# Optimization experiments

Measured on AMD Instinct MI355X. Metric: run time of the kernel, lower is better.

## Reference

```python
import jax, jax.numpy as jnp
import numpy as np

CONF_THRESH = 0.05      # confidence_threshold
IOU_THRESH = 0.15       # nms_iou_threshold
MAX_PER_CLASS = 550     # max_detection_per_class
MAX_TOTAL = 1100        # max_detection
NEG = -1e9              # sentinel for suppressed / below-threshold scores


def _to_corners(b):
    # convert_to_min_max_corner: (cx, cy, w, h) -> (x1, y1, x2, y2)
    xy, wh = b[..., :2], b[..., 2:4]
    return jnp.concatenate([xy - wh * 0.5, xy + wh * 0.5], axis=-1)


def _area(b):
    return jnp.clip(b[..., 2] - b[..., 0], 0.0) * jnp.clip(b[..., 3] - b[..., 1], 0.0)


def _iou_one_many(box, boxes):
    # box: [4], boxes: [N,4] in corner format
    lt = jnp.maximum(box[:2], boxes[:, :2])
    rb = jnp.minimum(box[2:], boxes[:, 2:])
    wh = jnp.clip(rb - lt, 0.0)
    inter = wh[:, 0] * wh[:, 1]
    union = _area(box) + _area(boxes) - inter
    return inter / jnp.maximum(union, 1e-8)


def _nms_single(boxes, scores):
    # Exact greedy hard-NMS for one (image, class): boxes [N,4], scores [N]
    s0 = jnp.where(scores > CONF_THRESH, scores, NEG)

    def step(s, _):
        i = jnp.argmax(s)
        sc = s[i]
        suppress = _iou_one_many(boxes[i], boxes) > IOU_THRESH
        ns = jnp.where(suppress, NEG, s).at[i].set(NEG)
        return ns, (i, sc)

    _, (sel_idx, sel_score) = jax.lax.scan(step, s0, None, length=MAX_PER_CLASS)
    return sel_idx, sel_score  # [K], [K]


def _decode(predictions):
    boxes = _to_corners(predictions[:, :, :4])          # [B,N,4]
    cls_probs = jax.nn.sigmoid(predictions[:, :, 4:])   # [B,N,C]
    scores = jnp.transpose(cls_probs, (0, 2, 1))        # [B,C,N]

    nms = jax.vmap(jax.vmap(_nms_single, in_axes=(None, 0)), in_axes=(0, 0))
    sel_idx, sel_score = nms(boxes, scores)             # [B,C,K]
    B, C, K = sel_score.shape

    gboxes = jnp.take_along_axis(boxes[:, None, :, :], sel_idx[..., None], axis=2)  # [B,C,K,4]
    classes = jnp.broadcast_to(jnp.arange(C, dtype=jnp.float32)[None, :, None], (B, C, K))

    fb = gboxes.reshape(B, C * K, 4)
    fs = sel_score.reshape(B, C * K)
    fc = classes.reshape(B, C * K)

    k = min(MAX_TOTAL, C * K)
    top_s, top_i = jax.lax.top_k(fs, k)                 # combined cross-class top-k
    tb = jnp.take_along_axis(fb, top_i[..., None], axis=1)
    tc = jnp.take_along_axis(fc, top_i, axis=1)

    valid = top_s > 0.5 * NEG                           # real detections have score in (conf, 1]
    nmsed_boxes = jnp.where(valid[..., None], tb, 0.0)
    nmsed_scores = jnp.where(valid, top_s, 0.0)
    nmsed_classes = jnp.where(valid, tc, 0.0)
    valid_detections = jnp.sum(valid, axis=1).astype(jnp.int32)
    return nmsed_boxes, nmsed_scores, nmsed_classes, valid_detections


def setup_inputs() -> dict:
    key = jax.random.key(0)
    k1, k2, k3 = jax.random.split(key, 3)
    B, N, C, IMG = 4, 49104, 2, 512.0
    u = jax.random.uniform(k1, (B, N, 4), dtype=jnp.float32)
    cxcy = u[..., :2] * IMG                  # centers within the image
    wh = 16.0 + u[..., 2:] * 128.0           # plausible anchor-ish sizes
    logits = jax.random.normal(k2, (B, N, C), dtype=jnp.float32) * 1.5 - 3.0
    predictions = jnp.concatenate([cxcy, wh, logits], axis=-1)  # [B,N,6]
    images = jax.random.uniform(k3, (B, 512, 512, 3), dtype=jnp.float32)
    return {"images": images, "predictions": predictions}


def reference(images, predictions):
    # images is accepted (as in the Keras layer) but unused by the math
    return _decode(predictions)
```

## Files before the change

### kernel.cpp

```cpp
#include <hip/hip_runtime.h>
#include <stdint.h>

#define NEGV    (-1000000000.0f)
#define CONF    0.05f
#define MAXSEL  550
#define CAP     32768
#define HEAD    1024
#define HW      (HEAD / 64)
#define NBINS   4096
#define BINBASE 0xC07F0000u
#define GCAP    3072
#define NSEG    64
#define TROUNDS 3

typedef unsigned long long u64;
typedef unsigned int u32;

__device__ __forceinline__ float areaf(float4 b) {
    return __fmul_rn(fmaxf(__fsub_rn(b.z, b.x), 0.0f), fmaxf(__fsub_rn(b.w, b.y), 0.0f));
}

__device__ __forceinline__ bool iou_gt2(float4 a, float aA, float4 b, float aB) {
    float ltx = fmaxf(a.x, b.x), lty = fmaxf(a.y, b.y);
    float rbx = fminf(a.z, b.z), rby = fminf(a.w, b.w);
    float wx = fmaxf(__fsub_rn(rbx, ltx), 0.0f);
    float wy = fmaxf(__fsub_rn(rby, lty), 0.0f);
    float inter = __fmul_rn(wx, wy);
    float uni = fmaxf(__fsub_rn(__fadd_rn(aA, aB), inter), 1e-8f);
    const double M = (double)0.15f + 0x1p-27;
    return (double)inter > M * (double)uni;
}

__device__ __forceinline__ u32 binof(u32 keyhi) {
    u32 bin = (keyhi - BINBASE) >> 14;
    return bin > (NBINS - 1) ? (NBINS - 1) : bin;
}

__global__ void k_decode(const float* __restrict__ pred, float4* __restrict__ boxes,
                         u32* __restrict__ hist, u32* __restrict__ llen,
                         u32* __restrict__ S_arr, u32* __restrict__ Sold,
                         int BN, int NBC) {
    int t = blockIdx.x * 256 + threadIdx.x;
    if (t < 2 * NBC * NBINS) hist[t] = 0;
    if (t < 2 * NBC) llen[t] = 0;
    if (t < NBC) { S_arr[t] = 0; Sold[t] = 0; }
    if (t >= BN) return;
    const float* p = pred + (size_t)t * 6;
    float cx = p[0], cy = p[1], w = p[2], h = p[3];
    float hw = __fmul_rn(w, 0.5f), hh = __fmul_rn(h, 0.5f);
    float4 b;
    b.x = __fsub_rn(cx, hw);
    b.y = __fsub_rn(cy, hh);
    b.z = __fadd_rn(cx, hw);
    b.w = __fadd_rn(cy, hh);
    boxes[t] = b;
}

__global__ __launch_bounds__(256) void k_hist(const float* __restrict__ pred,
                                              u32* __restrict__ hist,
                                              u64* __restrict__ L0,
                                              u32* __restrict__ llen0,
                                              int Nn, int Cc, int TIL) {
    int bt = blockIdx.x;
    int tile = bt % TIL, bc = bt / TIL;
    int b = bc / Cc, c = bc % Cc;
    int n = tile * 256 + threadIdx.x;
    bool p = false; u32 hi = 0;
    if (n < Nn) {
        float lg = pred[((size_t)b * Nn + n) * 6 + 4 + c];
        float sc = __fdiv_rn(1.0f, __fadd_rn(1.0f, expf(-lg)));
        if (sc > CONF) {
            p = true;
            hi = ~__float_as_uint(sc);
            atomicAdd(&hist[bc * NBINS + binof(hi)], 1u);
        }
    }
    u64 bal = __ballot(p);
    __shared__ u32 wb[4]; __shared__ u32 base;
    int lane = threadIdx.x & 63, wv = threadIdx.x >> 6;
    if (lane == 0) wb[wv] = (u32)__popcll(bal);
    __syncthreads();
    if (threadIdx.x == 0) {
        u32 run = 0;
        for (int q = 0; q < 4; ++q) { u32 v = wb[q]; wb[q] = run; run += v; }
        base = run ? atomicAdd(&llen0[bc], run) : 0u;
    }
    __syncthreads();
    if (p) {
        u32 pos = base + wb[wv] + (u32)__popcll(bal & ((1ull << lane) - 1ull));
        if (pos < CAP)
            L0[(size_t)bc * CAP + pos] = ((u64)hi << 32) | (u32)n;
    }
}

__global__ __launch_bounds__(1024) void k_headsort(const u64* __restrict__ list,
                                                   const u32* __restrict__ llen_cur,
                                                   const u32* __restrict__ hc,
                                                   u32* __restrict__ hn,
                                                   u32* __restrict__ ln,
                                                   const float4* __restrict__ boxes,
                                                   const u32* __restrict__ S_arr,
                                                   u64* __restrict__ headkey,
                                                   float4* __restrict__ headbox,
                                                   float* __restrict__ headarea,
                                                   u32* __restrict__ hl_arr,
                                                   u64* __restrict__ hmax_arr,
                                                   int Nn, int Cc) {
    int bc = blockIdx.x, b = bc / Cc;
    int tid = threadIdx.x, lane = tid & 63, wv = tid >> 6;
    __shared__ u64 buf[4096];
    __shared__ u32 gcnt;
    __shared__ int s_t;
    for (int i = tid; i < NBINS; i += 1024) hn[bc * NBINS + i] = 0;
    if (tid == 0) { ln[bc] = 0; gcnt = 0; }
    __syncthreads();
    if ((int)S_arr[bc] >= MAXSEL) { if (tid == 0) hl_arr[bc] = 0; return; }
    int len = (int)llen_cur[bc]; if (len > CAP) len = CAP;
    if (wv == 0) {
        if (lane == 0) s_t = -1;
        const u32* h = hc + bc * NBINS;
        int base = lane * 64;
        u32 s = 0;
        for (int i = 0; i < 64; ++i) s += h[base + i];
        u32 p = s;
        for (int d = 1; d < 64; d <<= 1) { u32 o = __shfl_up(p, d); if (lane >= d) p += o; }
        u32 total = __shfl(p, 63);
        u32 K = total < HEAD ? total : HEAD;
        if (K > 0) {
            u64 bal = __ballot(p >= K);
            int tl = (int)__builtin_ctzll(bal);
            if (lane == tl) {
                u32 cum = p - s;
                for (int i = 0; i < 64; ++i) {
                    cum += h[base + i];
                    if (cum >= K) {
                        s_t = (cum <= GCAP) ? (base + i) : (base + i - 1);
                        break;
                    }
                }
            }
        }
    }
    __syncthreads();
    int t = s_t;
    if (t >= 0) {
        const u64* src = list + (size_t)bc * CAP;
        for (int i = tid; i < len; i += 1024) {
            u64 key = src[i];
            if ((int)binof((u32)(key >> 32)) <= t) {
                u32 pos = atomicAdd(&gcnt, 1u);
                if (pos < GCAP) buf[pos] = key;
            }
        }
    }
    __syncthreads();
    int g = (int)gcnt; if (g > GCAP) g = GCAP;
    int SN = 1; while (SN < g) SN <<= 1;
    for (int i = g + tid; i < SN; i += 1024) buf[i] = ~0ull;
    __syncthreads();
    for (int k = 2; k <= SN; k <<= 1) {
        for (int j = k >> 1; j > 0; j >>= 1) {
            for (int idx = tid; idx < SN / 2; idx += 1024) {
                int i = ((idx & ~(j - 1)) << 1) | (idx & (j - 1));
                int q = i | j;
                bool up = ((i & k) == 0);
                u64 x = buf[i], y = buf[q];
                if ((x > y) == up) { buf[i] = y; buf[q] = x; }
            }
            __syncthreads();
        }
    }
    int hl = g < HEAD ? g : HEAD;
    if (tid == 0) { hl_arr[bc] = (u32)hl; hmax_arr[bc] = hl > 0 ? buf[hl - 1] : 0ull; }
    for (int i = tid; i < hl; i += 1024) {
        u64 key = buf[i];
        headkey[bc * HEAD + i] = key;
        float4 bx = boxes[(size_t)b * Nn + (u32)key];
        headbox[bc * HEAD + i] = bx;
        headarea[bc * HEAD + i] = areaf(bx);
    }
}

__global__ __launch_bounds__(256) void k_premask(const float4* __restrict__ headbox,
                                                 const float* __restrict__ headarea,
                                                 const u32* __restrict__ hl_arr,
                                                 u64* __restrict__ masks) {
    int blk = blockIdx.x, bc = blk >> 4, rb = blk & 15;
    int hl = (int)hl_arr[bc];
    if (hl <= 0) return;
    __shared__ float4 chB[HEAD];
    __shared__ float  chA[HEAD];
    for (int i = threadIdx.x; i < hl; i += 256) {
        chB[i] = headbox[bc * HEAD + i];
        chA[i] = headarea[bc * HEAD + i];
    }
    __syncthreads();
    int r = (rb << 6) + (threadIdx.x & 63);
    int part = threadIdx.x >> 6;
    if (r >= hl) return;
    float4 a = chB[r]; float aA = chA[r];
    u64* row = masks + ((size_t)bc * HEAD + r) * HW;
    for (int w = part * 4; w < part * 4 + 4; ++w) {
        u64 bits = 0;
        int cb = w << 6;
        int j1 = hl - cb; if (j1 > 64) j1 = 64;
        int j0 = (cb > r) ? 0 : (r + 1 - cb);
        for (int j = j0; j < j1; ++j)
            if (iou_gt2(a, aA, chB[cb + j], chA[cb + j])) bits |= (1ull << j);
        row[w] = bits;
    }
}

__global__ __launch_bounds__(1024) void k_chain(const u64* __restrict__ headkey,
                                                const u32* __restrict__ hl_arr,
                                                const u64* __restrict__ masks,
                                                const float4* __restrict__ headbox,
                                                const float* __restrict__ headarea,
                                                u32* __restrict__ sel_n,
                                                float* __restrict__ sel_s,
                                                float4* __restrict__ selb_g,
                                                float* __restrict__ sela_g,
                                                u32* __restrict__ S_arr,
                                                u32* __restrict__ Sold) {
    int bc = blockIdx.x;
    int tid = threadIdx.x, lane = tid & 63;
    __shared__ u64 mrow[HEAD * HW];
    __shared__ u64 kky[HEAD];
    __shared__ u32 selidx[MAXSEL];
    __shared__ int s_S;
    int S0 = (int)S_arr[bc];
    if (tid == 0) Sold[bc] = (u32)S0;
    int hl = (int)hl_arr[bc];
    if (hl <= 0 || S0 >= MAXSEL) return;
    const u64* gm = masks + (size_t)bc * HEAD * HW;
    for (int i = tid; i < hl * HW; i += 1024) mrow[i] = gm[i];
    for (int i = tid; i < hl; i += 1024) kky[i] = headkey[bc * HEAD + i];
    __syncthreads();
    if (tid < 64) {
        u64 rem = ~0ull;
        if (lane < HW) {
            int lo = lane << 6;
            rem = (hl >= lo + 64) ? 0ull : (hl <= lo ? ~0ull : ~((1ull << (hl - lo)) - 1ull));
        }
        int S = S0;
        while (S < MAXSEL) {
            bool av = (lane < HW) && (rem != ~0ull);
            u64 bal = __ballot(av);
            if (!bal) break;
            int w0 = (int)__builtin_ctzll(bal);
            u64 nz = __shfl((u64)(~rem), w0);
            int kz = (int)__builtin_ctzll(nz);
            int i = (w0 << 6) + kz;
            if (lane == 0) selidx[S] = (u32)i;
            if (lane < HW) rem |= mrow[i * HW + lane];
            if (lane == w0) rem |= (1ull << kz);
            ++S;
        }
        if (lane == 0) { s_S = S; S_arr[bc] = (u32)S; }
    }
    __syncthreads();
    int S = s_S;
    for (int s = S0 + tid; s < S; s += 1024) {
        u32 i = selidx[s];
        u64 k64 = kky[i];
        sel_n[bc * MAXSEL + s] = (u32)k64;
        sel_s[bc * MAXSEL + s] = __uint_as_float(~(u32)(k64 >> 32));
        selb_g[bc * MAXSEL + s] = headbox[bc * HEAD + i];
        sela_g[bc * MAXSEL + s] = headarea[bc * HEAD + i];
    }
}

__global__ __launch_bounds__(256) void k_mark(const float4* __restrict__ boxes,
                                              const u64* __restrict__ Lc,
                                              const u32* __restrict__ llen_c,
                                              const float4* __restrict__ selb_g,
                                              const float* __restrict__ sela_g,
                                              const u32* __restrict__ S_arr,
                                              const u32* __restrict__ Sold,
                                              const u64* __restrict__ hmax_arr,
                                              const u32* __restrict__ hl_arr,
                                              u64* __restrict__ Ln,
                                              u32* __restrict__ llen_n,
                                              u32* __restrict__ hist_n,
                                              int Nn, int Cc) {
    int blk = blockIdx.x, bc = blk / NSEG, seg = blk % NSEG;
    int tid = threadIdx.x, lane = tid & 63, wv = tid >> 6;
    int b = bc / Cc;
    int S0 = (int)Sold[bc], S1 = (int)S_arr[bc];
    if (S1 >= MAXSEL) return;
    int len = (int)llen_c[bc]; if (len > CAP) len = CAP;
    if (len <= 0) return;
    int ns = S1 - S0;
    u64 hmax = ((int)hl_arr[bc] > 0) ? hmax_arr[bc] : 0ull;
    __shared__ float4 sb[MAXSEL];
    __shared__ float  sa[MAXSEL];
    for (int s = tid; s < ns; s += 256) {
        sb[s] = selb_g[bc * MAXSEL + S0 + s];
        sa[s] = sela_g[bc * MAXSEL + S0 + s];
    }
    __syncthreads();
    __shared__ u32 wb[4]; __shared__ u32 base;
    int chunk = (len + NSEG - 1) / NSEG;
    int lo = seg * chunk, hi2 = lo + chunk; if (hi2 > len) hi2 = len;
    const u64* src = Lc + (size_t)bc * CAP;
    u64* dst = Ln + (size_t)bc * CAP;
    for (int st = lo; st < hi2; st += 256) {
        int i = st + tid;
        bool alive = i < hi2; u64 key = 0;
        if (alive) {
            key = src[i];
            if (key <= hmax) alive = false;
            else {
                float4 bx = boxes[(size_t)b * Nn + (u32)key];
                float aA = areaf(bx);
                for (int s = 0; s < ns; ++s)
                    if (iou_gt2(bx, aA, sb[s], sa[s])) { alive = false; break; }
            }
        }
        u64 bal = __ballot(alive);
        if (lane == 0) wb[wv] = (u32)__popcll(bal);
        __syncthreads();
        if (tid == 0) {
            u32 run = 0;
            for (int q = 0; q < 4; ++q) { u32 v = wb[q]; wb[q] = run; run += v; }
            base = run ? atomicAdd(&llen_n[bc], run) : 0u;
        }
        __syncthreads();
        if (alive) {
            u32 pos = base + wb[wv] + (u32)__popcll(bal & ((1ull << lane) - 1ull));
            if (pos < CAP) dst[pos] = key;
            atomicAdd(&hist_n[bc * NBINS + binof((u32)(key >> 32))], 1u);
        }
        __syncthreads();
    }
}

__global__ __launch_bounds__(1024) void k_final(const u32* __restrict__ selcnt,
                                                const u32* __restrict__ sel_n,
                                                const float* __restrict__ sel_s,
                                                const float4* __restrict__ boxes,
                                                float* __restrict__ out,
                                                int Nn, int Cc, int Bb) {
    int b = blockIdx.x, tid = threadIdx.x;
    const int TOT = MAXSEL * 2;
    __shared__ u64 sk[2048];
    u32 c0 = selcnt[b * Cc + 0];
    u32 c1 = selcnt[b * Cc + 1];
    for (int t = tid; t < 2048; t += 1024) {
        u64 key;
        if (t < TOT) {
            int c = t / MAXSEL, k2 = t % MAXSEL;
            u32 cc = (c == 0) ? c0 : c1;
            float sc = (k2 < (int)cc) ? sel_s[(size_t)(b * Cc + c) * MAXSEL + k2] : NEGV;
            u32 u = __float_as_uint(sc);
            u32 ord = (u & 0x80000000u) ? ~u : (u | 0x80000000u);
            key = (((u64)(~ord)) << 32) | (u32)t;
        } else {
            key = ~0ull;
        }
        sk[t] = key;
    }
    __syncthreads();
    for (int k = 2; k <= 2048; k <<= 1) {
        for (int j = k >> 1; j > 0; j >>= 1) {
            int idx = tid;
            int i = ((idx & ~(j - 1)) << 1) | (idx & (j - 1));
            int p = i | j;
            bool up = ((i & k) == 0);
            u64 x = sk[i], y = sk[p];
            if ((x > y) == up) { sk[i] = y; sk[p] = x; }
            __syncthreads();
        }
    }
    int off_scores = Bb * TOT * 4;
    int off_classes = off_scores + Bb * TOT;
    int off_valid = off_classes + Bb * TOT;
    for (int r = tid; r < TOT; r += 1024) {
        u64 key = sk[r];
        u32 flat = (u32)(key & 0xffffffffull);
        u32 hi = (u32)(key >> 32);
        u32 ord = ~hi;
        float sc = (ord & 0x80000000u) ? __uint_as_float(ord & 0x7fffffffu)
                                       : __uint_as_float(~ord);
        bool valid = sc > -5.0e8f;
        int c = (int)(flat / MAXSEL), k2 = (int)(flat % MAXSEL);
        float4 bxv = make_float4(0.f, 0.f, 0.f, 0.f);
        float so = 0.f, co = 0.f;
        if (valid) {
            u32 n = sel_n[(size_t)(b * Cc + c) * MAXSEL + k2];
            bxv = boxes[(size_t)b * Nn + n];
            so = sc;
            co = (float)c;
        }
        ((float4*)out)[b * TOT + r] = bxv;
        out[off_scores + b * TOT + r] = so;
        out[off_classes + b * TOT + r] = co;
    }
    if (tid == 0) out[off_valid + b] = (float)(c0 + c1);
}

extern "C" void kernel_launch(void* const* d_in, const int* in_sizes, int n_in,
                              void* d_out, int out_size, void* d_ws, size_t ws_size,
                              hipStream_t stream) {
    const float* pred = (const float*)d_in[1];
    float* out = (float*)d_out;
    int Bb = out_size / 6601;
    int Nn = in_sizes[1] / (6 * Bb);
    const int Cc = 2;
    if (Bb <= 0 || Nn <= 0) return;
    int NBC = Bb * Cc;
    int TIL = (Nn + 255) / 256;

    char* ws = (char*)d_ws;
    size_t off = 0;
    auto alloc = [&](size_t bytes) { void* p = ws + off; off = (off + bytes + 255) & ~(size_t)255; return p; };
    float4* boxes   = (float4*)alloc((size_t)Bb * Nn * 16);
    u64* L0         = (u64*)alloc((size_t)NBC * CAP * 8);
    u64* L1         = (u64*)alloc((size_t)NBC * CAP * 8);
    u32* hist       = (u32*)alloc(2 * (size_t)NBC * NBINS * 4);
    u32* llen       = (u32*)alloc(2 * NBC * 4);
    u64* headkey    = (u64*)alloc((size_t)NBC * HEAD * 8);
    float4* headbox = (float4*)alloc((size_t)NBC * HEAD * 16);
    float* headarea = (float*)alloc((size_t)NBC * HEAD * 4);
    u32* hl_arr     = (u32*)alloc(NBC * 4);
    u64* hmax_arr   = (u64*)alloc(NBC * 8);
    u32* sel_n      = (u32*)alloc((size_t)NBC * MAXSEL * 4);
    float* sel_s    = (float*)alloc((size_t)NBC * MAXSEL * 4);
    float4* selb_g  = (float4*)alloc((size_t)NBC * MAXSEL * 16);
    float* sela_g   = (float*)alloc((size_t)NBC * MAXSEL * 4);
    u32* S_arr      = (u32*)alloc(NBC * 4);
    u32* Sold       = (u32*)alloc(NBC * 4);
    u64* masks      = (u64*)alloc((size_t)NBC * HEAD * HW * 8);
    if (off > ws_size) return;

    int BN = Bb * Nn;
    k_decode<<<(BN + 255) / 256, 256, 0, stream>>>(pred, boxes, hist, llen, S_arr, Sold, BN, NBC);
    k_hist<<<NBC * TIL, 256, 0, stream>>>(pred, hist, L0, llen, Nn, Cc, TIL);

    for (int r = 0; r < TROUNDS; ++r) {
        int cur = r & 1, nxt = (r + 1) & 1;
        u64* Lc = cur ? L1 : L0;
        u64* Ln = nxt ? L1 : L0;
        u32* lc = llen + cur * NBC;
        u32* ln = llen + nxt * NBC;
        u32* hc = hist + (size_t)cur * NBC * NBINS;
        u32* hn = hist + (size_t)nxt * NBC * NBINS;
        k_headsort<<<NBC, 1024, 0, stream>>>(Lc, lc, hc, hn, ln, boxes, S_arr,
                                             headkey, headbox, headarea, hl_arr, hmax_arr, Nn, Cc);
        k_premask<<<NBC * 16, 256, 0, stream>>>(headbox, headarea, hl_arr, masks);
        k_chain<<<NBC, 1024, 0, stream>>>(headkey, hl_arr, masks, headbox, headarea,
                                          sel_n, sel_s, selb_g, sela_g, S_arr, Sold);
        if (r + 1 < TROUNDS)
            k_mark<<<NBC * NSEG, 256, 0, stream>>>(boxes, Lc, lc, selb_g, sela_g, S_arr, Sold,
                                                   hmax_arr, hl_arr, Ln, ln, hn, Nn, Cc);
    }
    k_final<<<Bb, 1024, 0, stream>>>(S_arr, sel_n, sel_s, boxes, out, Nn, Cc, Bb);
}
```

Baseline: 359.2 us.

## Fuse all NMS stages into one persistent cooperative kernel with grid syncs

Replaces the sequence of separate launches (decode, histogram, per-round headsort, premask, chain, mark, final) with a single cooperative mega-kernel of 256 blocks of 1024 threads. Stages are separated by grid.sync() and share a union of shared-memory buffers. The goal is to remove the launch overhead and inter-kernel gaps of about a dozen small launches. In exchange, the serial stages (sort, chain) run on only a few blocks while the rest of the grid waits at barriers. The large 1024-thread blocks with a big shared union may also limit occupancy.

After: 749.3 us. 109% more time.

```diff
diff --git a/kernel.cpp b/kernel.cpp
--- a/kernel.cpp
+++ b/kernel.cpp
@@ -1,20 +1,55 @@
 #include <hip/hip_runtime.h>
+#include <hip/hip_cooperative_groups.h>
 #include <stdint.h>
+
+namespace cg = cooperative_groups;
 
 #define NEGV    (-1000000000.0f)
 #define CONF    0.05f
 #define MAXSEL  550
 #define CAP     32768
 #define HEAD    1024
-#define HW      (HEAD / 64)
+#define HW      16
 #define NBINS   4096
 #define BINBASE 0xC07F0000u
 #define GCAP    3072
-#define NSEG    64
+#define NSEG    32
+#define GRID    256
 #define TROUNDS 3
 
 typedef unsigned long long u64;
 typedef unsigned int u32;
+
+struct Params {
+    const float* pred;
+    float* out;
+    float4* boxes;
+    u64* L0; u64* L1;
+    u32* hist;
+    u32* llen;
+    int* tbin;
+    u64* headkey;
+    float4* headbox;
+    float* headarea;
+    u32* hl_arr;
+    u64* hmax_arr;
+    u32* sel_n;
+    float* sel_s;
+    float4* selb_g;
+    float* sela_g;
+    u32* S_arr;
+    u32* Sold;
+    u64* masks;
+    int Bb, Nn, Cc, NBC, TIL4;
+};
+
+union SharedU {
+    struct { u64 mrow[HEAD * HW]; u64 kky[HEAD]; u32 selidx[MAXSEL]; } ch;
+    struct { u64 buf[4096]; } hs;
+    struct { float4 chB[HEAD]; float chA[HEAD]; } pm;
+    struct { float4 sb[MAXSEL]; float sa[MAXSEL]; } mk;
+    struct { u64 sk[2048]; } fn;
+};
 
 __device__ __forceinline__ float areaf(float4 b) {
     return __fmul_rn(fmaxf(__fsub_rn(b.z, b.x), 0.0f), fmaxf(__fsub_rn(b.w, b.y), 0.0f));
@@ -36,367 +71,343 @@
     return bin > (NBINS - 1) ? (NBINS - 1) : bin;
 }
 
-__global__ void k_decode(const float* __restrict__ pred, float4* __restrict__ boxes,
-                         u32* __restrict__ hist, u32* __restrict__ llen,
-                         u32* __restrict__ S_arr, u32* __restrict__ Sold,
-                         int BN, int NBC) {
-    int t = blockIdx.x * 256 + threadIdx.x;
-    if (t < 2 * NBC * NBINS) hist[t] = 0;
-    if (t < 2 * NBC) llen[t] = 0;
-    if (t < NBC) { S_arr[t] = 0; Sold[t] = 0; }
-    if (t >= BN) return;
-    const float* p = pred + (size_t)t * 6;
-    float cx = p[0], cy = p[1], w = p[2], h = p[3];
-    float hw = __fmul_rn(w, 0.5f), hh = __fmul_rn(h, 0.5f);
-    float4 b;
-    b.x = __fsub_rn(cx, hw);
-    b.y = __fsub_rn(cy, hh);
-    b.z = __fadd_rn(cx, hw);
-    b.w = __fadd_rn(cy, hh);
-    boxes[t] = b;
-}
-
-__global__ __launch_bounds__(256) void k_hist(const float* __restrict__ pred,
-                                              u32* __restrict__ hist,
-                                              u64* __restrict__ L0,
-                                              u32* __restrict__ llen0,
-                                              int Nn, int Cc, int TIL) {
-    int bt = blockIdx.x;
-    int tile = bt % TIL, bc = bt / TIL;
-    int b = bc / Cc, c = bc % Cc;
-    int n = tile * 256 + threadIdx.x;
-    bool p = false; u32 hi = 0;
-    if (n < Nn) {
-        float lg = pred[((size_t)b * Nn + n) * 6 + 4 + c];
-        float sc = __fdiv_rn(1.0f, __fadd_rn(1.0f, expf(-lg)));
-        if (sc > CONF) {
-            p = true;
-            hi = ~__float_as_uint(sc);
-            atomicAdd(&hist[bc * NBINS + binof(hi)], 1u);
-        }
+__global__ void __launch_bounds__(1024, 4) mega(Params P) {
+    cg::grid_group grid = cg::this_grid();
+    __shared__ SharedU sh;
+    __shared__ u32 s_wb[16];
+    __shared__ u32 s_base, s_gcnt;
+    __shared__ int s_S;
+
+    const int tid = threadIdx.x, lane = tid & 63, wv = tid >> 6;
+    const int gsz = gridDim.x * 1024;
+    const int gt0 = blockIdx.x * 1024 + tid;
+    const int NBC = P.NBC, Cc = P.Cc, Nn = P.Nn, Bb = P.Bb;
+
+    for (int t = gt0; t < 2 * NBC * NBINS; t += gsz) P.hist[t] = 0;
+    if (gt0 < 2 * NBC) P.llen[gt0] = 0;
+    if (gt0 < NBC) { P.S_arr[gt0] = 0; P.Sold[gt0] = 0; }
+    int BN = Bb * Nn;
+    for (int t = gt0; t < BN; t += gsz) {
+        const float* p = P.pred + (size_t)t * 6;
+        float cx = p[0], cy = p[1], w = p[2], h = p[3];
+        float hw = __fmul_rn(w, 0.5f), hh = __fmul_rn(h, 0.5f);
+        float4 b;
+        b.x = __fsub_rn(cx, hw);
+        b.y = __fsub_rn(cy, hh);
+        b.z = __fadd_rn(cx, hw);
+        b.w = __fadd_rn(cy, hh);
+        P.boxes[t] = b;
     }
-    u64 bal = __ballot(p);
-    __shared__ u32 wb[4]; __shared__ u32 base;
-    int lane = threadIdx.x & 63, wv = threadIdx.x >> 6;
-    if (lane == 0) wb[wv] = (u32)__popcll(bal);
-    __syncthreads();
-    if (threadIdx.x == 0) {
-        u32 run = 0;
-        for (int q = 0; q < 4; ++q) { u32 v = wb[q]; wb[q] = run; run += v; }
-        base = run ? atomicAdd(&llen0[bc], run) : 0u;
-    }
-    __syncthreads();
-    if (p) {
-        u32 pos = base + wb[wv] + (u32)__popcll(bal & ((1ull << lane) - 1ull));
-        if (pos < CAP)
-            L0[(size_t)bc * CAP + pos] = ((u64)hi << 32) | (u32)n;
-    }
-}
-
-__global__ __launch_bounds__(1024) void k_headsort(const u64* __restrict__ list,
-                                                   const u32* __restrict__ llen_cur,
-                                                   const u32* __restrict__ hc,
-                                                   u32* __restrict__ hn,
-                                                   u32* __restrict__ ln,
-                                                   const float4* __restrict__ boxes,
-                                                   const u32* __restrict__ S_arr,
-                                                   u64* __restrict__ headkey,
-                                                   float4* __restrict__ headbox,
-                                                   float* __restrict__ headarea,
-                                                   u32* __restrict__ hl_arr,
-                                                   u64* __restrict__ hmax_arr,
-                                                   int Nn, int Cc) {
-    int bc = blockIdx.x, b = bc / Cc;
-    int tid = threadIdx.x, lane = tid & 63, wv = tid >> 6;
-    __shared__ u64 buf[4096];
-    __shared__ u32 gcnt;
-    __shared__ int s_t;
-    for (int i = tid; i < NBINS; i += 1024) hn[bc * NBINS + i] = 0;
-    if (tid == 0) { ln[bc] = 0; gcnt = 0; }
-    __syncthreads();
-    if ((int)S_arr[bc] >= MAXSEL) { if (tid == 0) hl_arr[bc] = 0; return; }
-    int len = (int)llen_cur[bc]; if (len > CAP) len = CAP;
-    if (wv == 0) {
-        if (lane == 0) s_t = -1;
-        const u32* h = hc + bc * NBINS;
-        int base = lane * 64;
-        u32 s = 0;
-        for (int i = 0; i < 64; ++i) s += h[base + i];
-        u32 p = s;
-        for (int d = 1; d < 64; d <<= 1) { u32 o = __shfl_up(p, d); if (lane >= d) p += o; }
-        u32 total = __shfl(p, 63);
-        u32 K = total < HEAD ? total : HEAD;
-        if (K > 0) {
-            u64 bal = __ballot(p >= K);
-            int tl = (int)__builtin_ctzll(bal);
-            if (lane == tl) {
-                u32 cum = p - s;
-                for (int i = 0; i < 64; ++i) {
-                    cum += h[base + i];
-                    if (cum >= K) {
-                        s_t = (cum <= GCAP) ? (base + i) : (base + i - 1);
-                        break;
-                    }
-                }
-            }
-        }
-    }
-    __syncthreads();
-    int t = s_t;
-    if (t >= 0) {
-        const u64* src = list + (size_t)bc * CAP;
-        for (int i = tid; i < len; i += 1024) {
-            u64 key = src[i];
-            if ((int)binof((u32)(key >> 32)) <= t) {
-                u32 pos = atomicAdd(&gcnt, 1u);
-                if (pos < GCAP) buf[pos] = key;
-            }
-        }
-    }
-    __syncthreads();
-    int g = (int)gcnt; if (g > GCAP) g = GCAP;
-    int SN = 1; while (SN < g) SN <<= 1;
-    for (int i = g + tid; i < SN; i += 1024) buf[i] = ~0ull;
-    __syncthreads();
-    for (int k = 2; k <= SN; k <<= 1) {
-        for (int j = k >> 1; j > 0; j >>= 1) {
-            for (int idx = tid; idx < SN / 2; idx += 1024) {
-                int i = ((idx & ~(j - 1)) << 1) | (idx & (j - 1));
-                int q = i | j;
-                bool up = ((i & k) == 0);
-                u64 x = buf[i], y = buf[q];
-                if ((x > y) == up) { buf[i] = y; buf[q] = x; }
-            }
-            __syncthreads();
-        }
-    }
-    int hl = g < HEAD ? g : HEAD;
-    if (tid == 0) { hl_arr[bc] = (u32)hl; hmax_arr[bc] = hl > 0 ? buf[hl - 1] : 0ull; }
-    for (int i = tid; i < hl; i += 1024) {
-        u64 key = buf[i];
-        headkey[bc * HEAD + i] = key;
-        float4 bx = boxes[(size_t)b * Nn + (u32)key];
-        headbox[bc * HEAD + i] = bx;
-        headarea[bc * HEAD + i] = areaf(bx);
-    }
-}
-
-__global__ __launch_bounds__(256) void k_premask(const float4* __restrict__ headbox,
-                                                 const float* __restrict__ headarea,
-                                                 const u32* __restrict__ hl_arr,
-                                                 u64* __restrict__ masks) {
-    int blk = blockIdx.x, bc = blk >> 4, rb = blk & 15;
-    int hl = (int)hl_arr[bc];
-    if (hl <= 0) return;
-    __shared__ float4 chB[HEAD];
-    __shared__ float  chA[HEAD];
-    for (int i = threadIdx.x; i < hl; i += 256) {
-        chB[i] = headbox[bc * HEAD + i];
-        chA[i] = headarea[bc * HEAD + i];
-    }
-    __syncthreads();
-    int r = (rb << 6) + (threadIdx.x & 63);
-    int part = threadIdx.x >> 6;
-    if (r >= hl) return;
-    float4 a = chB[r]; float aA = chA[r];
-    u64* row = masks + ((size_t)bc * HEAD + r) * HW;
-    for (int w = part * 4; w < part * 4 + 4; ++w) {
-        u64 bits = 0;
-        int cb = w << 6;
-        int j1 = hl - cb; if (j1 > 64) j1 = 64;
-        int j0 = (cb > r) ? 0 : (r + 1 - cb);
-        for (int j = j0; j < j1; ++j)
-            if (iou_gt2(a, aA, chB[cb + j], chA[cb + j])) bits |= (1ull << j);
-        row[w] = bits;
-    }
-}
-
-__global__ __launch_bounds__(1024) void k_chain(const u64* __restrict__ headkey,
-                                                const u32* __restrict__ hl_arr,
-                                                const u64* __restrict__ masks,
-                                                const float4* __restrict__ headbox,
-                                                const float* __restrict__ headarea,
-                                                u32* __restrict__ sel_n,
-                                                float* __restrict__ sel_s,
-                                                float4* __restrict__ selb_g,
-                                                float* __restrict__ sela_g,
-                                                u32* __restrict__ S_arr,
-                                                u32* __restrict__ Sold) {
-    int bc = blockIdx.x;
-    int tid = threadIdx.x, lane = tid & 63;
-    __shared__ u64 mrow[HEAD * HW];
-    __shared__ u64 kky[HEAD];
-    __shared__ u32 selidx[MAXSEL];
-    __shared__ int s_S;
-    int S0 = (int)S_arr[bc];
-    if (tid == 0) Sold[bc] = (u32)S0;
-    int hl = (int)hl_arr[bc];
-    if (hl <= 0 || S0 >= MAXSEL) return;
-    const u64* gm = masks + (size_t)bc * HEAD * HW;
-    for (int i = tid; i < hl * HW; i += 1024) mrow[i] = gm[i];
-    for (int i = tid; i < hl; i += 1024) kky[i] = headkey[bc * HEAD + i];
-    __syncthreads();
-    if (tid < 64) {
-        u64 rem = ~0ull;
-        if (lane < HW) {
-            int lo = lane << 6;
-            rem = (hl >= lo + 64) ? 0ull : (hl <= lo ? ~0ull : ~((1ull << (hl - lo)) - 1ull));
-        }
-        int S = S0;
-        while (S < MAXSEL) {
-            bool av = (lane < HW) && (rem != ~0ull);
-            u64 bal = __ballot(av);
-            if (!bal) break;
-            int w0 = (int)__builtin_ctzll(bal);
-            u64 nz = __shfl((u64)(~rem), w0);
-            int kz = (int)__builtin_ctzll(nz);
-            int i = (w0 << 6) + kz;
-            if (lane == 0) selidx[S] = (u32)i;
-            if (lane < HW) rem |= mrow[i * HW + lane];
-            if (lane == w0) rem |= (1ull << kz);
-            ++S;
-        }
-        if (lane == 0) { s_S = S; S_arr[bc] = (u32)S; }
-    }
-    __syncthreads();
-    int S = s_S;
-    for (int s = S0 + tid; s < S; s += 1024) {
-        u32 i = selidx[s];
-        u64 k64 = kky[i];
-        sel_n[bc * MAXSEL + s] = (u32)k64;
-        sel_s[bc * MAXSEL + s] = __uint_as_float(~(u32)(k64 >> 32));
-        selb_g[bc * MAXSEL + s] = headbox[bc * HEAD + i];
-        sela_g[bc * MAXSEL + s] = headarea[bc * HEAD + i];
-    }
-}
-
-__global__ __launch_bounds__(256) void k_mark(const float4* __restrict__ boxes,
-                                              const u64* __restrict__ Lc,
-                                              const u32* __restrict__ llen_c,
-                                              const float4* __restrict__ selb_g,
-                                              const float* __restrict__ sela_g,
-                                              const u32* __restrict__ S_arr,
-                                              const u32* __restrict__ Sold,
-                                              const u64* __restrict__ hmax_arr,
-                                              const u32* __restrict__ hl_arr,
-                                              u64* __restrict__ Ln,
-                                              u32* __restrict__ llen_n,
-                                              u32* __restrict__ hist_n,
-                                              int Nn, int Cc) {
-    int blk = blockIdx.x, bc = blk / NSEG, seg = blk % NSEG;
-    int tid = threadIdx.x, lane = tid & 63, wv = tid >> 6;
-    int b = bc / Cc;
-    int S0 = (int)Sold[bc], S1 = (int)S_arr[bc];
-    if (S1 >= MAXSEL) return;
-    int len = (int)llen_c[bc]; if (len > CAP) len = CAP;
-    if (len <= 0) return;
-    int ns = S1 - S0;
-    u64 hmax = ((int)hl_arr[bc] > 0) ? hmax_arr[bc] : 0ull;
-    __shared__ float4 sb[MAXSEL];
-    __shared__ float  sa[MAXSEL];
-    for (int s = tid; s < ns; s += 256) {
-        sb[s] = selb_g[bc * MAXSEL + S0 + s];
-        sa[s] = sela_g[bc * MAXSEL + S0 + s];
-    }
-    __syncthreads();
-    __shared__ u32 wb[4]; __shared__ u32 base;
-    int chunk = (len + NSEG - 1) / NSEG;
-    int lo = seg * chunk, hi2 = lo + chunk; if (hi2 > len) hi2 = len;
-    const u64* src = Lc + (size_t)bc * CAP;
-    u64* dst = Ln + (size_t)bc * CAP;
-    for (int st = lo; st < hi2; st += 256) {
-        int i = st + tid;
-        bool alive = i < hi2; u64 key = 0;
-        if (alive) {
-            key = src[i];
-            if (key <= hmax) alive = false;
-            else {
-                float4 bx = boxes[(size_t)b * Nn + (u32)key];
-                float aA = areaf(bx);
-                for (int s = 0; s < ns; ++s)
-                    if (iou_gt2(bx, aA, sb[s], sa[s])) { alive = false; break; }
-            }
-        }
-        u64 bal = __ballot(alive);
-        if (lane == 0) wb[wv] = (u32)__popcll(bal);
+    grid.sync();
+
+    for (int bt = blockIdx.x; bt < NBC * P.TIL4; bt += gridDim.x) {
+        int tile = bt % P.TIL4, bc = bt / P.TIL4;
+        int b = bc / Cc, c = bc % Cc;
+        int n = tile * 1024 + tid;
+        bool pz = false; u32 hi = 0;
+        if (n < Nn) {
+            float lg = P.pred[((size_t)b * Nn + n) * 6 + 4 + c];
+            float sc = __fdiv_rn(1.0f, __fadd_rn(1.0f, expf(-lg)));
+            if (sc > CONF) {
+                pz = true;
+                hi = ~__float_as_uint(sc);
+                atomicAdd(&P.hist[bc * NBINS + binof(hi)], 1u);
+            }
+        }
+        u64 bal = __ballot(pz);
+        if (lane == 0) s_wb[wv] = (u32)__popcll(bal);
         __syncthreads();
         if (tid == 0) {
             u32 run = 0;
-            for (int q = 0; q < 4; ++q) { u32 v = wb[q]; wb[q] = run; run += v; }
-            base = run ? atomicAdd(&llen_n[bc], run) : 0u;
+            for (int q = 0; q < 16; ++q) { u32 v = s_wb[q]; s_wb[q] = run; run += v; }
+            s_base = run ? atomicAdd(&P.llen[bc], run) : 0u;
         }
         __syncthreads();
-        if (alive) {
-            u32 pos = base + wb[wv] + (u32)__popcll(bal & ((1ull << lane) - 1ull));
-            if (pos < CAP) dst[pos] = key;
-            atomicAdd(&hist_n[bc * NBINS + binof((u32)(key >> 32))], 1u);
+        if (pz) {
+            u32 pos = s_base + s_wb[wv] + (u32)__popcll(bal & ((1ull << lane) - 1ull));
+            if (pos < CAP) P.L0[(size_t)bc * CAP + pos] = ((u64)hi << 32) | (u32)n;
         }
         __syncthreads();
     }
-}
-
-__global__ __launch_bounds__(1024) void k_final(const u32* __restrict__ selcnt,
-                                                const u32* __restrict__ sel_n,
-                                                const float* __restrict__ sel_s,
-                                                const float4* __restrict__ boxes,
-                                                float* __restrict__ out,
-                                                int Nn, int Cc, int Bb) {
-    int b = blockIdx.x, tid = threadIdx.x;
-    const int TOT = MAXSEL * 2;
-    __shared__ u64 sk[2048];
-    u32 c0 = selcnt[b * Cc + 0];
-    u32 c1 = selcnt[b * Cc + 1];
-    for (int t = tid; t < 2048; t += 1024) {
-        u64 key;
-        if (t < TOT) {
-            int c = t / MAXSEL, k2 = t % MAXSEL;
-            u32 cc = (c == 0) ? c0 : c1;
-            float sc = (k2 < (int)cc) ? sel_s[(size_t)(b * Cc + c) * MAXSEL + k2] : NEGV;
-            u32 u = __float_as_uint(sc);
-            u32 ord = (u & 0x80000000u) ? ~u : (u | 0x80000000u);
-            key = (((u64)(~ord)) << 32) | (u32)t;
-        } else {
-            key = ~0ull;
-        }
-        sk[t] = key;
+    grid.sync();
+
+    for (int r = 0; r < TROUNDS; ++r) {
+        const u64* Lc = (r & 1) ? P.L1 : P.L0;
+        u64* Ln = (r & 1) ? P.L0 : P.L1;
+        const u32* lc = P.llen + (r & 1) * NBC;
+        u32* ln = P.llen + ((r + 1) & 1) * NBC;
+        const u32* hc = P.hist + (size_t)(r & 1) * NBC * NBINS;
+        u32* hn = P.hist + (size_t)((r + 1) & 1) * NBC * NBINS;
+
+        if (blockIdx.x == 0) {
+            for (int i = tid; i < NBC * NBINS; i += 1024) hn[i] = 0;
+            if (tid < NBC) ln[tid] = 0;
+            if (wv < NBC) {
+                const u32* h = hc + wv * NBINS;
+                int base = lane * 64;
+                u32 s = 0;
+                for (int i = 0; i < 64; ++i) s += h[base + i];
+                u32 p = s;
+                for (int d = 1; d < 64; d <<= 1) { u32 o = __shfl_up(p, d); if (lane >= d) p += o; }
+                u32 total = __shfl(p, 63);
+                u32 K = total < HEAD ? total : HEAD;
+                if (K > 0) {
+                    u64 bal = __ballot(p >= K);
+                    int tl = (int)__builtin_ctzll(bal);
+                    if (lane == tl) {
+                        u32 cum = p - s;
+                        for (int i = 0; i < 64; ++i) {
+                            cum += h[base + i];
+                            if (cum >= K) {
+                                P.tbin[wv] = (cum <= GCAP) ? (base + i) : (base + i - 1);
+                                break;
+                            }
+                        }
+                    }
+                } else if (lane == 0) P.tbin[wv] = -1;
+            }
+        }
+        grid.sync();
+
+        if (blockIdx.x < NBC) {
+            int bc = blockIdx.x, b = bc / Cc;
+            if (tid == 0) s_gcnt = 0;
+            __syncthreads();
+            if ((int)P.S_arr[bc] >= MAXSEL) {
+                if (tid == 0) P.hl_arr[bc] = 0;
+            } else {
+                int t = P.tbin[bc];
+                int len = (int)lc[bc]; if (len > CAP) len = CAP;
+                if (t >= 0) {
+                    const u64* src = Lc + (size_t)bc * CAP;
+                    for (int i = tid; i < len; i += 1024) {
+                        u64 key = src[i];
+                        if ((int)binof((u32)(key >> 32)) <= t) {
+                            u32 pos = atomicAdd(&s_gcnt, 1u);
+                            if (pos < GCAP) sh.hs.buf[pos] = key;
+                        }
+                    }
+                }
+                __syncthreads();
+                int g = (int)s_gcnt; if (g > GCAP) g = GCAP;
+                int SN = 1; while (SN < g) SN <<= 1;
+                for (int i = g + tid; i < SN; i += 1024) sh.hs.buf[i] = ~0ull;
+                __syncthreads();
+                for (int k = 2; k <= SN; k <<= 1) {
+                    for (int j = k >> 1; j > 0; j >>= 1) {
+                        for (int idx = tid; idx < SN / 2; idx += 1024) {
+                            int i2 = ((idx & ~(j - 1)) << 1) | (idx & (j - 1));
+                            int q = i2 | j;
+                            bool up = ((i2 & k) == 0);
+                            u64 x = sh.hs.buf[i2], y = sh.hs.buf[q];
+                            if ((x > y) == up) { sh.hs.buf[i2] = y; sh.hs.buf[q] = x; }
+                        }
+                        __syncthreads();
+                    }
+                }
+                int hl = g < HEAD ? g : HEAD;
+                if (tid == 0) {
+                    P.hl_arr[bc] = (u32)hl;
+                    P.hmax_arr[bc] = hl > 0 ? sh.hs.buf[hl - 1] : 0ull;
+                }
+                for (int i = tid; i < hl; i += 1024) {
+                    u64 key = sh.hs.buf[i];
+                    P.headkey[bc * HEAD + i] = key;
+                    float4 bx = P.boxes[(size_t)b * Nn + (u32)key];
+                    P.headbox[bc * HEAD + i] = bx;
+                    P.headarea[bc * HEAD + i] = areaf(bx);
+                }
+            }
+        }
+        grid.sync();
+
+        if (blockIdx.x < NBC * 16) {
+            int bc = blockIdx.x >> 4, rb = blockIdx.x & 15;
+            int hl = (int)P.hl_arr[bc];
+            if (hl > 0) {
+                for (int i = tid; i < hl; i += 1024) {
+                    sh.pm.chB[i] = P.headbox[bc * HEAD + i];
+                    sh.pm.chA[i] = P.headarea[bc * HEAD + i];
+                }
+                __syncthreads();
+                if (tid < 256) {
+                    int r2 = (rb << 6) + (tid & 63);
+                    int part = tid >> 6;
+                    if (r2 < hl) {
+                        float4 a = sh.pm.chB[r2]; float aA = sh.pm.chA[r2];
+                        u64* row = P.masks + ((size_t)bc * HEAD + r2) * HW;
+                        for (int w = part * 4; w < part * 4 + 4; ++w) {
+                            u64 bits = 0;
+                            int cb = w << 6;
+                            int j1 = hl - cb; if (j1 > 64) j1 = 64;
+                            int j0 = (cb > r2) ? 0 : (r2 + 1 - cb);
+                            for (int j = j0; j < j1; ++j)
+                                if (iou_gt2(a, aA, sh.pm.chB[cb + j], sh.pm.chA[cb + j]))
+                                    bits |= (1ull << j);
+                            row[w] = bits;
+                        }
+                    }
+                }
+            }
+        }
+        grid.sync();
+
+        if (blockIdx.x < NBC) {
+            int bc = blockIdx.x;
+            int S0 = (int)P.S_arr[bc];
+            if (tid == 0) P.Sold[bc] = (u32)S0;
+            int hl = (int)P.hl_arr[bc];
+            if (hl > 0 && S0 < MAXSEL) {
+                const u64* gm = P.masks + (size_t)bc * HEAD * HW;
+                for (int i = tid; i < hl * HW; i += 1024) sh.ch.mrow[i] = gm[i];
+                for (int i = tid; i < hl; i += 1024) sh.ch.kky[i] = P.headkey[bc * HEAD + i];
+                __syncthreads();
+                if (tid < 64) {
+                    u64 rem = ~0ull;
+                    if (lane < HW) {
+                        int lo = lane << 6;
+                        rem = (hl >= lo + 64) ? 0ull
+                              : (hl <= lo ? ~0ull : ~((1ull << (hl - lo)) - 1ull));
+                    }
+                    int S = S0;
+                    while (S < MAXSEL) {
+                        bool av = (lane < HW) && (rem != ~0ull);
+                        u64 bal = __ballot(av);
+                        if (!bal) break;
+                        int w0 = (int)__builtin_ctzll(bal);
+                        u64 nz = __shfl((u64)(~rem), w0);
+                        int kz = (int)__builtin_ctzll(nz);
+                        int i2 = (w0 << 6) + kz;
+                        if (lane == 0) sh.ch.selidx[S] = (u32)i2;
+                        if (lane < HW) rem |= sh.ch.mrow[i2 * HW + lane];
+                        if (lane == w0) rem |= (1ull << kz);
+                        ++S;
+                    }
+                    if (lane == 0) { s_S = S; P.S_arr[bc] = (u32)S; }
+                }
+                __syncthreads();
+                int S = s_S;
+                for (int s = S0 + tid; s < S; s += 1024) {
+                    u32 i2 = sh.ch.selidx[s];
+                    u64 k64 = sh.ch.kky[i2];
+                    P.sel_n[bc * MAXSEL + s] = (u32)k64;
+                    P.sel_s[bc * MAXSEL + s] = __uint_as_float(~(u32)(k64 >> 32));
+                    P.selb_g[bc * MAXSEL + s] = P.headbox[bc * HEAD + i2];
+                    P.sela_g[bc * MAXSEL + s] = P.headarea[bc * HEAD + i2];
+                }
+            }
+        }
+        grid.sync();
+
+        if (r + 1 < TROUNDS) {
+            if (blockIdx.x < NBC * NSEG) {
+                int bc = blockIdx.x / NSEG, seg = blockIdx.x % NSEG;
+                int b = bc / Cc;
+                int S0 = (int)P.Sold[bc], S1 = (int)P.S_arr[bc];
+                int len = (int)lc[bc]; if (len > CAP) len = CAP;
+                if (S1 < MAXSEL && len > 0) {
+                    int ns = S1 - S0;
+                    u64 hmax = ((int)P.hl_arr[bc] > 0) ? P.hmax_arr[bc] : 0ull;
+                    for (int s = tid; s < ns; s += 1024) {
+                        sh.mk.sb[s] = P.selb_g[bc * MAXSEL + S0 + s];
+                        sh.mk.sa[s] = P.sela_g[bc * MAXSEL + S0 + s];
+                    }
+                    __syncthreads();
+                    int chunk = (len + NSEG - 1) / NSEG;
+                    int lo = seg * chunk, hi2 = lo + chunk; if (hi2 > len) hi2 = len;
+                    const u64* src = Lc + (size_t)bc * CAP;
+                    u64* dst = Ln + (size_t)bc * CAP;
+                    for (int st = lo; st < hi2; st += 1024) {
+                        int i = st + tid;
+                        bool alive = i < hi2; u64 key = 0;
+                        if (alive) {
+                            key = src[i];
+                            if (key <= hmax) alive = false;
+                            else {
+                                float4 bx = P.boxes[(size_t)b * Nn + (u32)key];
+                                float aA = areaf(bx);
+                                for (int s = 0; s < ns; ++s)
+                                    if (iou_gt2(bx, aA, sh.mk.sb[s], sh.mk.sa[s])) { alive = false; break; }
+                            }
+                        }
+                        u64 bal = __ballot(alive);
+                        if (lane == 0) s_wb[wv] = (u32)__popcll(bal);
+                        __syncthreads();
+                        if (tid == 0) {
+                            u32 run = 0;
+                            for (int q = 0; q < 16; ++q) { u32 v = s_wb[q]; s_wb[q] = run; run += v; }
+                            s_base = run ? atomicAdd(&ln[bc], run) : 0u;
+                        }
+                        __syncthreads();
+                        if (alive) {
+                            u32 pos = s_base + s_wb[wv] + (u32)__popcll(bal & ((1ull << lane) - 1ull));
+                            if (pos < CAP) dst[pos] = key;
+                            atomicAdd(&hn[bc * NBINS + binof((u32)(key >> 32))], 1u);
+                        }
+                        __syncthreads();
+                    }
+                }
+            }
+            grid.sync();
+        }
     }
-    __syncthreads();
-    for (int k = 2; k <= 2048; k <<= 1) {
-        for (int j = k >> 1; j > 0; j >>= 1) {
-            int idx = tid;
-            int i = ((idx & ~(j - 1)) << 1) | (idx & (j - 1));
-            int p = i | j;
-            bool up = ((i & k) == 0);
-            u64 x = sk[i], y = sk[p];
-            if ((x > y) == up) { sk[i] = y; sk[p] = x; }
-            __syncthreads();
-        }
+
+    if (blockIdx.x < Bb) {
+        int b = blockIdx.x;
+        const int TOT = MAXSEL * 2;
+        u32 c0 = P.S_arr[b * Cc + 0];
+        u32 c1 = P.S_arr[b * Cc + 1];
+        for (int t = tid; t < 2048; t += 1024) {
+            u64 key;
+            if (t < TOT) {
+                int c = t / MAXSEL, k2 = t % MAXSEL;
+                u32 cc = (c == 0) ? c0 : c1;
+                float sc = (k2 < (int)cc) ? P.sel_s[(size_t)(b * Cc + c) * MAXSEL + k2] : NEGV;
+                u32 u = __float_as_uint(sc);
+                u32 ord = (u & 0x80000000u) ? ~u : (u | 0x80000000u);
+                key = (((u64)(~ord)) << 32) | (u32)t;
+            } else {
+                key = ~0ull;
+            }
+            sh.fn.sk[t] = key;
+        }
+        __syncthreads();
+        for (int k = 2; k <= 2048; k <<= 1) {
+            for (int j = k >> 1; j > 0; j >>= 1) {
+                int i = ((tid & ~(j - 1)) << 1) | (tid & (j - 1));
+                int p = i | j;
+                bool up = ((i & k) == 0);
+                u64 x = sh.fn.sk[i], y = sh.fn.sk[p];
+                if ((x > y) == up) { sh.fn.sk[i] = y; sh.fn.sk[p] = x; }
+                __syncthreads();
+            }
+        }
+        int off_scores = Bb * TOT * 4;
+        int off_classes = off_scores + Bb * TOT;
+        int off_valid = off_classes + Bb * TOT;
+        for (int r = tid; r < TOT; r += 1024) {
+            u64 key = sh.fn.sk[r];
+            u32 flat = (u32)(key & 0xffffffffull);
+            u32 hi = (u32)(key >> 32);
+            u32 ord = ~hi;
+            float sc = (ord & 0x80000000u) ? __uint_as_float(ord & 0x7fffffffu)
+                                           : __uint_as_float(~ord);
+            bool valid = sc > -5.0e8f;
+            int c = (int)(flat / MAXSEL), k2 = (int)(flat % MAXSEL);
+            float4 bxv = make_float4(0.f, 0.f, 0.f, 0.f);
+            float so = 0.f, co = 0.f;
+            if (valid) {
+                u32 n = P.sel_n[(size_t)(b * Cc + c) * MAXSEL + k2];
+                bxv = P.boxes[(size_t)b * Nn + n];
+                so = sc;
+                co = (float)c;
+            }
+            ((float4*)P.out)[b * TOT + r] = bxv;
+            P.out[off_scores + b * TOT + r] = so;
+            P.out[off_classes + b * TOT + r] = co;
+        }
+        if (tid == 0) P.out[off_valid + b] = (float)(c0 + c1);
     }
-    int off_scores = Bb * TOT * 4;
-    int off_classes = off_scores + Bb * TOT;
-    int off_valid = off_classes + Bb * TOT;
-    for (int r = tid; r < TOT; r += 1024) {
-        u64 key = sk[r];
-        u32 flat = (u32)(key & 0xffffffffull);
-        u32 hi = (u32)(key >> 32);
-        u32 ord = ~hi;
-        float sc = (ord & 0x80000000u) ? __uint_as_float(ord & 0x7fffffffu)
-                                       : __uint_as_float(~ord);
-        bool valid = sc > -5.0e8f;
-        int c = (int)(flat / MAXSEL), k2 = (int)(flat % MAXSEL);
-        float4 bxv = make_float4(0.f, 0.f, 0.f, 0.f);
-        float so = 0.f, co = 0.f;
-        if (valid) {
-            u32 n = sel_n[(size_t)(b * Cc + c) * MAXSEL + k2];
-            bxv = boxes[(size_t)b * Nn + n];
-            so = sc;
-            co = (float)c;
-        }
-        ((float4*)out)[b * TOT + r] = bxv;
-        out[off_scores + b * TOT + r] = so;
-        out[off_classes + b * TOT + r] = co;
-    }
-    if (tid == 0) out[off_valid + b] = (float)(c0 + c1);
 }
 
 extern "C" void kernel_launch(void* const* d_in, const int* in_sizes, int n_in,
@@ -409,50 +420,34 @@
     const int Cc = 2;
     if (Bb <= 0 || Nn <= 0) return;
     int NBC = Bb * Cc;
-    int TIL = (Nn + 255) / 256;
+    int TIL4 = (Nn + 1023) / 1024;
 
     char* ws = (char*)d_ws;
     size_t off = 0;
     auto alloc = [&](size_t bytes) { void* p = ws + off; off = (off + bytes + 255) & ~(size_t)255; return p; };
-    float4* boxes   = (float4*)alloc((size_t)Bb * Nn * 16);
-    u64* L0         = (u64*)alloc((size_t)NBC * CAP * 8);
-    u64* L1         = (u64*)alloc((size_t)NBC * CAP * 8);
-    u32* hist       = (u32*)alloc(2 * (size_t)NBC * NBINS * 4);
-    u32* llen       = (u32*)alloc(2 * NBC * 4);
-    u64* headkey    = (u64*)alloc((size_t)NBC * HEAD * 8);
-    float4* headbox = (float4*)alloc((size_t)NBC * HEAD * 16);
-    float* headarea = (float*)alloc((size_t)NBC * HEAD * 4);
-    u32* hl_arr     = (u32*)alloc(NBC * 4);
-    u64* hmax_arr   = (u64*)alloc(NBC * 8);
-    u32* sel_n      = (u32*)alloc((size_t)NBC * MAXSEL * 4);
-    float* sel_s    = (float*)alloc((size_t)NBC * MAXSEL * 4);
-    float4* selb_g  = (float4*)alloc((size_t)NBC * MAXSEL * 16);
-    float* sela_g   = (float*)alloc((size_t)NBC * MAXSEL * 4);
-    u32* S_arr      = (u32*)alloc(NBC * 4);
-    u32* Sold       = (u32*)alloc(NBC * 4);
-    u64* masks      = (u64*)alloc((size_t)NBC * HEAD * HW * 8);
+    Params P;
+    P.pred = pred; P.out = out;
+    P.boxes    = (float4*)alloc((size_t)Bb * Nn * 16);
+    P.L0       = (u64*)alloc((size_t)NBC * CAP * 8);
+    P.L1       = (u64*)alloc((size_t)NBC * CAP * 8);
+    P.hist     = (u32*)alloc(2 * (size_t)NBC * NBINS * 4);
+    P.llen     = (u32*)alloc(2 * NBC * 4);
+    P.tbin     = (int*)alloc(NBC * 4);
+    P.headkey  = (u64*)alloc((size_t)NBC * HEAD * 8);
+    P.headbox  = (float4*)alloc((size_t)NBC * HEAD * 16);
+    P.headarea = (float*)alloc((size_t)NBC * HEAD * 4);
+    P.hl_arr   = (u32*)alloc(NBC * 4);
+    P.hmax_arr = (u64*)alloc(NBC * 8);
+    P.sel_n    = (u32*)alloc((size_t)NBC * MAXSEL * 4);
+    P.sel_s    = (float*)alloc((size_t)NBC * MAXSEL * 4);
+    P.selb_g   = (float4*)alloc((size_t)NBC * MAXSEL * 16);
+    P.sela_g   = (float*)alloc((size_t)NBC * MAXSEL * 4);
+    P.S_arr    = (u32*)alloc(NBC * 4);
+    P.Sold     = (u32*)alloc(NBC * 4);
+    P.masks    = (u64*)alloc((size_t)NBC * HEAD * HW * 8);
     if (off > ws_size) return;
-
-    int BN = Bb * Nn;
-    k_decode<<<(BN + 255) / 256, 256, 0, stream>>>(pred, boxes, hist, llen, S_arr, Sold, BN, NBC);
-    k_hist<<<NBC * TIL, 256, 0, stream>>>(pred, hist, L0, llen, Nn, Cc, TIL);
-
-    for (int r = 0; r < TROUNDS; ++r) {
-        int cur = r & 1, nxt = (r + 1) & 1;
-        u64* Lc = cur ? L1 : L0;
-        u64* Ln = nxt ? L1 : L0;
-        u32* lc = llen + cur * NBC;
-        u32* ln = llen + nxt * NBC;
-        u32* hc = hist + (size_t)cur * NBC * NBINS;
-        u32* hn = hist + (size_t)nxt * NBC * NBINS;
-        k_headsort<<<NBC, 1024, 0, stream>>>(Lc, lc, hc, hn, ln, boxes, S_arr,
-                                             headkey, headbox, headarea, hl_arr, hmax_arr, Nn, Cc);
-        k_premask<<<NBC * 16, 256, 0, stream>>>(headbox, headarea, hl_arr, masks);
-        k_chain<<<NBC, 1024, 0, stream>>>(headkey, hl_arr, masks, headbox, headarea,
-                                          sel_n, sel_s, selb_g, sela_g, S_arr, Sold);
-        if (r + 1 < TROUNDS)
-            k_mark<<<NBC * NSEG, 256, 0, stream>>>(boxes, Lc, lc, selb_g, sela_g, S_arr, Sold,
-                                                   hmax_arr, hl_arr, Ln, ln, hn, Nn, Cc);
-    }
-    k_final<<<Bb, 1024, 0, stream>>>(S_arr, sel_n, sel_s, boxes, out, Nn, Cc, Bb);
+    P.Bb = Bb; P.Nn = Nn; P.Cc = Cc; P.NBC = NBC; P.TIL4 = TIL4;
+
+    void* kargs[] = { (void*)&P };
+    hipLaunchCooperativeKernel((const void*)mega, dim3(GRID), dim3(1024), kargs, 0, stream);
 }
```
